# Kernel optimization log

Measured on AMD Instinct MI355X. Metric: run time of the kernel, lower is better.

The kernel has to match this reference:

```python
import jax, jax.numpy as jnp
import numpy as np

DIM = 1024
DIM_HEAD = 64
HEADS = 8
MULT = 4
ATTN_INNER = HEADS * DIM_HEAD            # 512
FF_INNER = MULT * DIM                    # 4096
FUSED = ATTN_INNER + DIM_HEAD + DIM_HEAD + 2 * FF_INNER  # 8832


def setup_inputs() -> dict:
    key = jax.random.key(0)
    ks = jax.random.split(key, 5)
    x = jax.random.normal(ks[0], (2, 2048, DIM), dtype=jnp.float32)
    gamma = jnp.ones((DIM,), dtype=jnp.float32)
    # Linear weights stored as [in, out]
    w_fused = jax.random.normal(ks[1], (DIM, FUSED), dtype=jnp.float32) * (DIM ** -0.5)
    w_attn_out = jax.random.normal(ks[2], (ATTN_INNER, DIM), dtype=jnp.float32) * (ATTN_INNER ** -0.5)
    w_ff_out = jax.random.normal(ks[3], (FF_INNER, DIM), dtype=jnp.float32) * (FF_INNER ** -0.5)
    return {"x": x, "gamma": gamma, "w_fused": w_fused,
            "w_attn_out": w_attn_out, "w_ff_out": w_ff_out}


def _forward(x, gamma, w_fused, w_attn_out, w_ff_out):
    b, n, d = x.shape
    # LayerNorm (beta buffer is zeros)
    mu = jnp.mean(x, axis=-1, keepdims=True)
    var = jnp.mean(jnp.square(x - mu), axis=-1, keepdims=True)
    xn = (x - mu) * jax.lax.rsqrt(var + 1e-5) * gamma
    # fused QKV + FF projection
    proj = jnp.einsum('bnd,df->bnf', xn, w_fused)
    q = proj[..., :ATTN_INNER]
    k = proj[..., ATTN_INNER:ATTN_INNER + DIM_HEAD]
    v = proj[..., ATTN_INNER + DIM_HEAD:ATTN_INNER + 2 * DIM_HEAD]
    ff = proj[..., ATTN_INNER + 2 * DIM_HEAD:]
    # multi-query attention: single shared K/V head of width DIM_HEAD
    q = q.reshape(b, n, HEADS, DIM_HEAD).transpose(0, 2, 1, 3) * (DIM_HEAD ** -0.5)
    sim = jnp.einsum('bhid,bjd->bhij', q, k)
    attn = jax.nn.softmax(sim, axis=-1)
    out = jnp.einsum('bhij,bjd->bhid', attn, v)
    out = out.transpose(0, 2, 1, 3).reshape(b, n, ATTN_INNER)
    attn_out = jnp.einsum('bna,ad->bnd', out, w_attn_out)
    # parallel SwiGLU FF: chunk -> (x_part, gate); silu(gate)*x_part
    ff_x, gate = ff[..., :FF_INNER], ff[..., FF_INNER:]
    ff_out = jnp.einsum('bnf,fd->bnd', jax.nn.silu(gate) * ff_x, w_ff_out)
    return attn_out + ff_out


def reference(x, gamma, w_fused, w_attn_out, w_ff_out):
    return _forward(x, gamma, w_fused, w_attn_out, w_ff_out)
```

## Files before the change

kernel.cpp:

```cpp
#include <hip/hip_runtime.h>
#include <hip/hip_bf16.h>
#include <stdint.h>

#define DIM     1024
#define SEQ     2048
#define NTOK    4096
#define HEADS   8
#define DH      64
#define AINNER  512
#define FFI     4096
#define FUSED   8832
#define HCOLS   4608

typedef __attribute__((ext_vector_type(8))) short short8;
typedef __attribute__((ext_vector_type(4))) short short4v;
typedef __attribute__((ext_vector_type(4))) float f32x4;

__device__ __forceinline__ short f2bf(float f) {
  union { float f; uint32_t u; } v; v.f = f;
  uint32_t r = v.u + 0x7fffu + ((v.u >> 16) & 1u);
  return (short)(r >> 16);
}
__device__ __forceinline__ float bf2f(short s) {
  union { uint32_t u; float f; } v; v.u = ((uint32_t)(uint16_t)s) << 16;
  return v.f;
}
__device__ __forceinline__ void g2l16(const void* g, void* l) {
  __builtin_amdgcn_global_load_lds((const __attribute__((address_space(1))) void*)g,
                                   (__attribute__((address_space(3))) void*)l, 16, 0, 0);
}

__global__ __launch_bounds__(256) void k_transpose_wf(const float* __restrict__ src,
                                                      short* __restrict__ dst) {
  __shared__ short tile[32][33];
  int c0 = blockIdx.x * 32;
  int r0 = blockIdx.y * 32;
  int tx = threadIdx.x & 31, ty = threadIdx.x >> 5;
#pragma unroll
  for (int i = 0; i < 32; i += 8)
    tile[ty + i][tx] = f2bf(src[(size_t)(r0 + ty + i) * FUSED + c0 + tx]);
  __syncthreads();
#pragma unroll
  for (int i = 0; i < 32; i += 8)
    dst[(size_t)(c0 + ty + i) * DIM + r0 + tx] = tile[tx][ty + i];
}

__global__ __launch_bounds__(256) void k_transpose_w2(const float* __restrict__ wao,
                                                      const float* __restrict__ wfo,
                                                      short* __restrict__ dst) {
  __shared__ short tile[32][33];
  int c0 = blockIdx.x * 32;
  int r0 = blockIdx.y * 32;
  int tx = threadIdx.x & 31, ty = threadIdx.x >> 5;
#pragma unroll
  for (int i = 0; i < 32; i += 8) {
    int r = r0 + ty + i;
    float v = (r < AINNER) ? wao[(size_t)r * DIM + c0 + tx]
                           : wfo[(size_t)(r - AINNER) * DIM + c0 + tx];
    tile[ty + i][tx] = f2bf(v);
  }
  __syncthreads();
#pragma unroll
  for (int i = 0; i < 32; i += 8)
    dst[(size_t)(c0 + ty + i) * HCOLS + r0 + tx] = tile[tx][ty + i];
}

__global__ __launch_bounds__(256) void k_ln(const float* __restrict__ x,
                                            const float* __restrict__ gamma,
                                            short* __restrict__ xn) {
  int row = blockIdx.x;
  int t = threadIdx.x;
  const float4* xr = (const float4*)(x + (size_t)row * DIM);
  float4 v = xr[t];
  float s = v.x + v.y + v.z + v.w;
  float s2 = v.x * v.x + v.y * v.y + v.z * v.z + v.w * v.w;
#pragma unroll
  for (int m = 1; m < 64; m <<= 1) { s += __shfl_xor(s, m); s2 += __shfl_xor(s2, m); }
  __shared__ float red[8];
  int w = t >> 6;
  if ((t & 63) == 0) { red[w] = s; red[4 + w] = s2; }
  __syncthreads();
  s = red[0] + red[1] + red[2] + red[3];
  s2 = red[4] + red[5] + red[6] + red[7];
  float mu = s * (1.f / DIM);
  float rs = rsqrtf(s2 * (1.f / DIM) - mu * mu + 1e-5f);
  const float4* g4 = (const float4*)gamma;
  float4 g = g4[t];
  short4v o;
  o.x = f2bf((v.x - mu) * rs * g.x);
  o.y = f2bf((v.y - mu) * rs * g.y);
  o.z = f2bf((v.z - mu) * rs * g.z);
  o.w = f2bf((v.w - mu) * rs * g.w);
  ((short4v*)(xn + (size_t)row * DIM))[t] = o;
}

template <int MODE, int BN>
__global__ __launch_bounds__(512, 2) void gemm8(const short* __restrict__ A, int lda,
                                                const short* __restrict__ Bt, int ldb,
                                                int K, void* __restrict__ out0,
                                                void* __restrict__ out1,
                                                void* __restrict__ out2,
                                                void* __restrict__ out3) {
  extern __shared__ __align__(16) short S[];
  constexpr int NFR = BN / 64;
  constexpr int BHALF = (BN == 256) ? 8192 : 4096;
  int tid = threadIdx.x, l = tid & 63, w = tid >> 6;
  int wm = w >> 2, wn = w & 3;
  int gx = gridDim.x, nwg = gx * gridDim.y;
  int hw = blockIdx.y * gx + blockIdx.x;
  int qq = nwg >> 3;
  int tile = (hw & 7) * qq + (hw >> 3);
  int bx = tile % gx, by = tile / gx;
  int mBase = by * 256, nBase = bx * BN;

  int srow = w * 8 + (l >> 3);
  int cs = (l & 7) ^ (l >> 3);
  const short* Ag = A + (size_t)(mBase + srow) * lda + cs * 8;
  const short* Bg = Bt + (size_t)(nBase + srow) * ldb + cs * 8;
  int dsto = w * 512 + l * 8;

#define STAGE_ALL(kt, db2)                                                      \
  {                                                                             \
    _Pragma("unroll") for (int h = 0; h < 2; ++h)                               \
        _Pragma("unroll") for (int s2 = 0; s2 < 2; ++s2)                        \
            g2l16(Ag + (size_t)(h * 128 + s2 * 64) * lda + (kt) * 64,           \
                  S + ((db2) * 2 + h) * 8192 + s2 * 4096 + dsto);               \
    if constexpr (BN == 256) {                                                  \
      _Pragma("unroll") for (int h = 0; h < 2; ++h)                             \
          _Pragma("unroll") for (int s2 = 0; s2 < 2; ++s2)                      \
              g2l16(Bg + (size_t)(h * 128 + s2 * 64) * ldb + (kt) * 64,         \
                    S + 32768 + ((db2) * 2 + h) * 8192 + s2 * 4096 + dsto);     \
    } else {                                                                    \
      _Pragma("unroll") for (int h = 0; h < 2; ++h)                             \
          g2l16(Bg + (size_t)(h * 64) * ldb + (kt) * 64,                        \
                S + 32768 + ((db2) * 2 + h) * 4096 + dsto);                     \
    }                                                                           \
  }

  int NT = K >> 6;
  STAGE_ALL(0, 0);

  int c0 = l & 15, kg = l >> 4, cx = l & 7;
  int brow = (wn & 1) * (BN / 4);
  f32x4 zero = {0.f, 0.f, 0.f, 0.f};
  f32x4 acc[8][NFR];
#pragma unroll
  for (int m = 0; m < 8; ++m)
#pragma unroll
    for (int n = 0; n < NFR; ++n) acc[m][n] = zero;

  for (int kt = 0; kt < NT; ++kt) {
    int db = kt & 1, dbn = db ^ 1;
    asm volatile("s_waitcnt vmcnt(0)\ns_barrier" ::: "memory");
    if (kt + 1 < NT) STAGE_ALL(kt + 1, dbn);
    const short* Ab = S + (db * 2 + wm) * 8192;
    const short* Bb = S + 32768 + (db * 2 + (wn >> 1)) * BHALF;
#pragma unroll
    for (int kkh = 0; kkh < 2; ++kkh) {
      int ch = (kkh * 4 + kg) ^ cx;
      short8 b[NFR], a[8];
#pragma unroll
      for (int n = 0; n < NFR; ++n)
        b[n] = *(const short8*)(Bb + (brow + n * 16 + c0) * 64 + ch * 8);
#pragma unroll
      for (int m = 0; m < 8; ++m)
        a[m] = *(const short8*)(Ab + (m * 16 + c0) * 64 + ch * 8);
      __builtin_amdgcn_s_setprio(1);
#pragma unroll
      for (int m = 0; m < 8; ++m)
#pragma unroll
        for (int n = 0; n < NFR; ++n)
          acc[m][n] = __builtin_amdgcn_mfma_f32_16x16x32_bf16(a[m], b[n], acc[m][n], 0, 0, 0);
      __builtin_amdgcn_s_setprio(0);
    }
  }
#undef STAGE_ALL

  int r0 = (l >> 4) * 4;
#pragma unroll
  for (int m = 0; m < 8; ++m)
#pragma unroll
    for (int n = 0; n < NFR; ++n)
#pragma unroll
      for (int r = 0; r < 4; ++r) {
        float val = acc[m][n][r];
        int row = mBase + wm * 128 + m * 16 + r0 + r;
        int col = nBase + wn * (BN / 4) + n * 16 + c0;
        if (MODE == 0) {
          if (col < AINNER)
            ((short*)out0)[(size_t)row * AINNER + col] = f2bf(val);
          else if (col < AINNER + DH)
            ((short*)out1)[(size_t)row * DH + (col - AINNER)] = f2bf(val);
          else if (col < AINNER + 2 * DH)
            ((short*)out2)[((size_t)(row >> 11) * DH + (col - AINNER - DH)) * SEQ +
                           (row & (SEQ - 1))] = f2bf(val);
          else
            ((short*)out3)[(size_t)row * HCOLS + AINNER + (col - 640)] = f2bf(val);
        } else {
          short* Hp = (short*)out0;
          size_t idx = (size_t)row * HCOLS + AINNER + col;
          float sg = val / (1.f + __expf(-val));
          Hp[idx] = f2bf(sg * bf2f(Hp[idx]));
        }
      }
}

__global__ __launch_bounds__(512, 2) void gemm_r(const short* __restrict__ A, int lda,
                                                 const short* __restrict__ Bt, int ldb,
                                                 int K, float* __restrict__ out0) {
  extern __shared__ __align__(16) short SA[];
  int tid = threadIdx.x, l = tid & 63, w = tid >> 6;
  int gx = gridDim.x;
  int nwg = gx * gridDim.y;
  int hw = blockIdx.y * gx + blockIdx.x;
  int qq = nwg >> 3;
  int tile = (hw & 7) * qq + (hw >> 3);
  int bx = tile % gx, by = tile / gx;
  int mBase = by * 128, nBase = bx * 128;

  int srow = w * 8 + (l >> 3);
  int cs = (l & 7) ^ (l >> 3);
  const short* Ag = A + (size_t)(mBase + srow) * lda + cs * 8;
  const short* Bg = Bt + (size_t)(nBase + srow) * ldb + cs * 8;
  short* ldsA = SA + w * 512 + l * 8;
  short* ldsB = ldsA + 8192;

  int NT = K >> 6;
  for (int tt = 0; tt < 3; ++tt) {
    int slot = tt & 3;
#pragma unroll
    for (int i = 0; i < 2; ++i) {
      g2l16(Ag + (size_t)(i * 64) * lda + tt * 64, ldsA + slot * 16384 + i * 4096);
      g2l16(Bg + (size_t)(i * 64) * ldb + tt * 64, ldsB + slot * 16384 + i * 4096);
    }
  }

  int wr = w >> 2, wc = w & 3;
  int c0 = l & 15, kg = l >> 4, cx = l & 7;
  f32x4 zero = {0.f, 0.f, 0.f, 0.f};
  f32x4 acc[4][2];
#pragma unroll
  for (int m = 0; m < 4; ++m)
#pragma unroll
    for (int n = 0; n < 2; ++n) acc[m][n] = zero;

  for (int kt = 0; kt < NT; ++kt) {
    if (kt + 2 < NT)      asm volatile("s_waitcnt vmcnt(8)\ns_barrier" ::: "memory");
    else if (kt + 1 < NT) asm volatile("s_waitcnt vmcnt(4)\ns_barrier" ::: "memory");
    else                  asm volatile("s_waitcnt vmcnt(0)\ns_barrier" ::: "memory");
    int slot = kt & 3;
    const short* Ab = SA + slot * 16384;
    const short* Bb = Ab + 8192;
    short8 af[4][2], bfr[2][2];
#pragma unroll
    for (int m = 0; m < 4; ++m)
#pragma unroll
      for (int kk = 0; kk < 2; ++kk)
        af[m][kk] = *(const short8*)(Ab + (wr * 64 + m * 16 + c0) * 64 + ((kk * 4 + kg) ^ cx) * 8);
#pragma unroll
    for (int n = 0; n < 2; ++n)
#pragma unroll
      for (int kk = 0; kk < 2; ++kk)
        bfr[n][kk] = *(const short8*)(Bb + (wc * 32 + n * 16 + c0) * 64 + ((kk * 4 + kg) ^ cx) * 8);
    int ts = kt + 3;
    if (ts < NT) {
      int s2 = ts & 3;
#pragma unroll
      for (int i = 0; i < 2; ++i) {
        g2l16(Ag + (size_t)(i * 64) * lda + ts * 64, ldsA + s2 * 16384 + i * 4096);
        g2l16(Bg + (size_t)(i * 64) * ldb + ts * 64, ldsB + s2 * 16384 + i * 4096);
      }
    }
    __builtin_amdgcn_s_setprio(1);
#pragma unroll
    for (int m = 0; m < 4; ++m)
#pragma unroll
      for (int n = 0; n < 2; ++n)
#pragma unroll
        for (int kk = 0; kk < 2; ++kk)
          acc[m][n] = __builtin_amdgcn_mfma_f32_16x16x32_bf16(af[m][kk], bfr[n][kk],
                                                              acc[m][n], 0, 0, 0);
    __builtin_amdgcn_s_setprio(0);
  }

  int r0 = (l >> 4) * 4;
#pragma unroll
  for (int m = 0; m < 4; ++m)
#pragma unroll
    for (int n = 0; n < 2; ++n)
#pragma unroll
      for (int r = 0; r < 4; ++r) {
        int row = mBase + wr * 64 + m * 16 + r0 + r;
        int col = nBase + wc * 32 + n * 16 + c0;
        out0[(size_t)row * DIM + col] = acc[m][n][r];
      }
}

__global__ __launch_bounds__(256) void k_attn(const short* __restrict__ qb,
                                              const short* __restrict__ kb,
                                              const short* __restrict__ vt,
                                              short* __restrict__ H) {
  __shared__ __align__(16) short Qs[64 * 64];
  __shared__ __align__(16) short Ks[128 * 64];
  __shared__ __align__(16) short Vs[64 * 128];
  __shared__ __align__(16) short Ps[4][16 * 128];
  int t = threadIdx.x, l = t & 63, w = t >> 6;
  int qt = blockIdx.x, bh = blockIdx.y;
  int b = bh >> 3, h = bh & 7;
  int q0 = qt * 64;

  int srow = w * 8 + (l >> 3);
  int schunk = (l & 7) ^ (l >> 3);
  {
    const short* Qg = qb + (size_t)(b * SEQ + q0 + srow) * AINNER + h * DH + schunk * 8;
    short* qs = Qs + w * 512 + l * 8;
#pragma unroll
    for (int i = 0; i < 2; ++i) g2l16(Qg + (size_t)(i * 32) * AINNER, qs + i * 2048);
  }
  const short* Kg = kb + (size_t)(b * SEQ + srow) * DH + schunk * 8;
  short* ksl = Ks + w * 512 + l * 8;
  int vrow = w * 4 + (l >> 4);
  int vchunk = (l & 15) ^ (vrow & 7);
  const short* Vg = vt + (size_t)b * DH * SEQ + (size_t)vrow * SEQ + vchunk * 8;
  short* vsl = Vs + w * 512 + l * 8;

#pragma unroll
  for (int i = 0; i < 4; ++i) {
    g2l16(Kg + (size_t)(i * 32) * DH, ksl + i * 2048);
    g2l16(Vg + (size_t)(i * 16) * SEQ, vsl + i * 2048);
  }

  float m_run[4], l_run[4];
  f32x4 zero = {0.f, 0.f, 0.f, 0.f};
  f32x4 Oacc[4];
#pragma unroll
  for (int r = 0; r < 4; ++r) { m_run[r] = -1e30f; l_run[r] = 0.f; }
#pragma unroll
  for (int n = 0; n < 4; ++n) Oacc[n] = zero;

  int c0 = l & 15, kg = l >> 4, cx = l & 7;
  short* pw = Ps[w];

  for (int kv0 = 0; kv0 < SEQ; kv0 += 128) {
    asm volatile("s_waitcnt vmcnt(0)\ns_barrier" ::: "memory");

    f32x4 sacc[8];
#pragma unroll
    for (int n = 0; n < 8; ++n) sacc[n] = zero;
#pragma unroll
    for (int kk = 0; kk < 2; ++kk) {
      int rr = w * 16 + c0;
      short8 aq = *(const short8*)(Qs + rr * 64 + ((kk * 4 + kg) ^ cx) * 8);
#pragma unroll
      for (int n = 0; n < 8; ++n) {
        int kr = n * 16 + c0;
        short8 bk = *(const short8*)(Ks + kr * 64 + ((kk * 4 + kg) ^ cx) * 8);
        sacc[n] = __builtin_amdgcn_mfma_f32_16x16x32_bf16(aq, bk, sacc[n], 0, 0, 0);
      }
    }
#pragma unroll
    for (int r = 0; r < 4; ++r) {
      float mx = -1e30f;
#pragma unroll
      for (int n = 0; n < 8; ++n) {
        sacc[n][r] *= 0.125f;
        mx = fmaxf(mx, sacc[n][r]);
      }
#pragma unroll
      for (int msk = 1; msk < 16; msk <<= 1) mx = fmaxf(mx, __shfl_xor(mx, msk));
      float nm = fmaxf(m_run[r], mx);
      float corr = __expf(m_run[r] - nm);
      m_run[r] = nm;
      float rs = 0.f;
#pragma unroll
      for (int n = 0; n < 8; ++n) {
        float p = __expf(sacc[n][r] - nm);
        sacc[n][r] = p;
        rs += p;
      }
#pragma unroll
      for (int msk = 1; msk < 16; msk <<= 1) rs += __shfl_xor(rs, msk);
      l_run[r] = l_run[r] * corr + rs;
      Oacc[0][r] *= corr; Oacc[1][r] *= corr; Oacc[2][r] *= corr; Oacc[3][r] *= corr;
    }
#pragma unroll
    for (int n = 0; n < 8; ++n)
#pragma unroll
      for (int r = 0; r < 4; ++r) {
        int pr = (l >> 4) * 4 + r;
        int pc = n * 16 + c0;
        pw[pr * 128 + ((pc >> 3) ^ (pr & 7)) * 8 + (pc & 7)] = f2bf(sacc[n][r]);
      }
    asm volatile("s_waitcnt lgkmcnt(0)" ::: "memory");
#pragma unroll
    for (int kk = 0; kk < 4; ++kk) {
      int pr = c0;
      short8 ap = *(const short8*)(pw + pr * 128 + ((kk * 4 + kg) ^ cx) * 8);
#pragma unroll
      for (int n = 0; n < 4; ++n) {
        int vr = n * 16 + c0;
        short8 bv = *(const short8*)(Vs + vr * 128 + ((kk * 4 + kg) ^ (vr & 7)) * 8);
        Oacc[n] = __builtin_amdgcn_mfma_f32_16x16x32_bf16(ap, bv, Oacc[n], 0, 0, 0);
      }
    }
    __syncthreads();
    int nx = kv0 + 128;
    if (nx < SEQ) {
#pragma unroll
      for (int i = 0; i < 4; ++i) {
        g2l16(Kg + (size_t)(nx + i * 32) * DH, ksl + i * 2048);
        g2l16(Vg + nx + (size_t)(i * 16) * SEQ, vsl + i * 2048);
      }
    }
  }
#pragma unroll
  for (int r = 0; r < 4; ++r) {
    float inv = 1.f / l_run[r];
    int row = b * SEQ + q0 + w * 16 + (l >> 4) * 4 + r;
#pragma unroll
    for (int n = 0; n < 4; ++n) {
      int col = h * DH + n * 16 + c0;
      H[(size_t)row * HCOLS + col] = f2bf(Oacc[n][r] * inv);
    }
  }
}

extern "C" void kernel_launch(void* const* d_in, const int* in_sizes, int n_in,
                              void* d_out, int out_size, void* d_ws, size_t ws_size,
                              hipStream_t stream) {
  const float* x     = (const float*)d_in[0];
  const float* gamma = (const float*)d_in[1];
  const float* w_f   = (const float*)d_in[2];
  const float* w_ao  = (const float*)d_in[3];
  const float* w_fo  = (const float*)d_in[4];
  float* out = (float*)d_out;

  char* ws = (char*)d_ws;
  size_t o = 0;
  short* WtF = (short*)(ws + o); o += (size_t)FUSED * DIM * 2;
  short* Wt2 = (short*)(ws + o); o += (size_t)DIM * HCOLS * 2;
  short* xn  = (short*)(ws + o); o += (size_t)NTOK * DIM * 2;
  short* qb  = (short*)(ws + o); o += (size_t)NTOK * AINNER * 2;
  short* kbf = (short*)(ws + o); o += (size_t)NTOK * DH * 2;
  short* vtb = (short*)(ws + o); o += (size_t)NTOK * DH * 2;
  short* H   = (short*)(ws + o); o += (size_t)NTOK * HCOLS * 2;

  k_transpose_wf<<<dim3(FUSED / 32, DIM / 32), 256, 0, stream>>>(w_f, WtF);
  k_transpose_w2<<<dim3(DIM / 32, HCOLS / 32), 256, 0, stream>>>(w_ao, w_fo, Wt2);
  k_ln<<<NTOK, 256, 0, stream>>>(x, gamma, xn);
  gemm8<0, 128><<<dim3(37, 16), 512, 98304, stream>>>(xn, DIM, WtF, DIM, DIM,
                                                      qb, kbf, vtb, H);
  k_attn<<<dim3(32, 16), 256, 0, stream>>>(qb, kbf, vtb, H);
  gemm8<1, 256><<<dim3(16, 16), 512, 131072, stream>>>(xn, DIM, WtF + (size_t)4736 * DIM, DIM,
                                                       DIM, H, nullptr, nullptr, nullptr);
  gemm_r<<<dim3(8, 32), 512, 131072, stream>>>(H, HCOLS, Wt2, HCOLS, HCOLS, out);
}
```

Measured before the change: 231.9 us.

## Fuse SwiGLU gate into projection GEMM and split-K the output GEMM

Measured after the change: 223.4 us. 3.7% less time.

```diff
diff --git a/kernel.cpp b/kernel.cpp
--- a/kernel.cpp
+++ b/kernel.cpp
@@ -94,115 +94,209 @@
   ((short4v*)(xn + (size_t)row * DIM))[t] = o;
 }
 
-template <int MODE, int BN>
-__global__ __launch_bounds__(512, 2) void gemm8(const short* __restrict__ A, int lda,
-                                                const short* __restrict__ Bt, int ldb,
-                                                int K, void* __restrict__ out0,
-                                                void* __restrict__ out1,
-                                                void* __restrict__ out2,
-                                                void* __restrict__ out3) {
+__global__ __launch_bounds__(512, 2) void p1(const short* __restrict__ A,
+                                             const short* __restrict__ Bt,
+                                             short* __restrict__ qb,
+                                             short* __restrict__ kbf,
+                                             short* __restrict__ vtb,
+                                             short* __restrict__ H) {
   extern __shared__ __align__(16) short S[];
-  constexpr int NFR = BN / 64;
-  constexpr int BHALF = (BN == 256) ? 8192 : 4096;
   int tid = threadIdx.x, l = tid & 63, w = tid >> 6;
   int wm = w >> 2, wn = w & 3;
-  int gx = gridDim.x, nwg = gx * gridDim.y;
-  int hw = blockIdx.y * gx + blockIdx.x;
-  int qq = nwg >> 3;
-  int tile = (hw & 7) * qq + (hw >> 3);
-  int bx = tile % gx, by = tile / gx;
-  int mBase = by * 256, nBase = bx * BN;
+  int hw = blockIdx.y * 37 + blockIdx.x;
+  int tile = (hw & 7) * 74 + (hw >> 3);
+  int bx = tile % 37, by = tile / 37;
+  int mBase = by * 256;
+  bool fused = bx < 32;
+  int b0row = fused ? (640 + bx * 128) : ((bx - 32) * 128);
+  int b1row = 4736 + bx * 128;
 
   int srow = w * 8 + (l >> 3);
   int cs = (l & 7) ^ (l >> 3);
-  const short* Ag = A + (size_t)(mBase + srow) * lda + cs * 8;
-  const short* Bg = Bt + (size_t)(nBase + srow) * ldb + cs * 8;
+  const short* Ag = A + (size_t)(mBase + srow) * DIM + cs * 8;
+  const short* Bg0 = Bt + (size_t)(b0row + srow) * DIM + cs * 8;
+  const short* Bg1 = Bt + (size_t)(b1row + srow) * DIM + cs * 8;
   int dsto = w * 512 + l * 8;
 
-#define STAGE_ALL(kt, db2)                                                      \
+#define P1_STAGE(kt, db)                                                        \
   {                                                                             \
-    _Pragma("unroll") for (int h = 0; h < 2; ++h)                               \
-        _Pragma("unroll") for (int s2 = 0; s2 < 2; ++s2)                        \
-            g2l16(Ag + (size_t)(h * 128 + s2 * 64) * lda + (kt) * 64,           \
-                  S + ((db2) * 2 + h) * 8192 + s2 * 4096 + dsto);               \
-    if constexpr (BN == 256) {                                                  \
-      _Pragma("unroll") for (int h = 0; h < 2; ++h)                             \
-          _Pragma("unroll") for (int s2 = 0; s2 < 2; ++s2)                      \
-              g2l16(Bg + (size_t)(h * 128 + s2 * 64) * ldb + (kt) * 64,         \
-                    S + 32768 + ((db2) * 2 + h) * 8192 + s2 * 4096 + dsto);     \
-    } else {                                                                    \
-      _Pragma("unroll") for (int h = 0; h < 2; ++h)                             \
-          g2l16(Bg + (size_t)(h * 64) * ldb + (kt) * 64,                        \
-                S + 32768 + ((db2) * 2 + h) * 4096 + dsto);                     \
+    _Pragma("unroll") for (int i = 0; i < 4; ++i)                               \
+        g2l16(Ag + (size_t)(i * 64) * DIM + (kt) * 64,                          \
+              S + (db) * 16384 + i * 4096 + dsto);                              \
+    _Pragma("unroll") for (int i = 0; i < 2; ++i)                               \
+        g2l16(Bg0 + (size_t)(i * 64) * DIM + (kt) * 64,                         \
+              S + 32768 + (db) * 16384 + i * 4096 + dsto);                      \
+    if (fused) {                                                                \
+      _Pragma("unroll") for (int i = 0; i < 2; ++i)                             \
+          g2l16(Bg1 + (size_t)(i * 64) * DIM + (kt) * 64,                       \
+                S + 32768 + (db) * 16384 + 8192 + i * 4096 + dsto);             \
     }                                                                           \
   }
 
-  int NT = K >> 6;
-  STAGE_ALL(0, 0);
+  const int NT = DIM / 64;
+  P1_STAGE(0, 0);
 
   int c0 = l & 15, kg = l >> 4, cx = l & 7;
-  int brow = (wn & 1) * (BN / 4);
   f32x4 zero = {0.f, 0.f, 0.f, 0.f};
-  f32x4 acc[8][NFR];
+  f32x4 accF[8][2], accG[8][2];
 #pragma unroll
   for (int m = 0; m < 8; ++m)
 #pragma unroll
-    for (int n = 0; n < NFR; ++n) acc[m][n] = zero;
+    for (int n = 0; n < 2; ++n) { accF[m][n] = zero; accG[m][n] = zero; }
 
   for (int kt = 0; kt < NT; ++kt) {
     int db = kt & 1, dbn = db ^ 1;
     asm volatile("s_waitcnt vmcnt(0)\ns_barrier" ::: "memory");
-    if (kt + 1 < NT) STAGE_ALL(kt + 1, dbn);
-    const short* Ab = S + (db * 2 + wm) * 8192;
-    const short* Bb = S + 32768 + (db * 2 + (wn >> 1)) * BHALF;
+    if (kt + 1 < NT) P1_STAGE(kt + 1, dbn);
+    const short* Ab = S + db * 16384;
+    const short* Bb = S + 32768 + db * 16384;
 #pragma unroll
     for (int kkh = 0; kkh < 2; ++kkh) {
-      int ch = (kkh * 4 + kg) ^ cx;
-      short8 b[NFR], a[8];
-#pragma unroll
-      for (int n = 0; n < NFR; ++n)
-        b[n] = *(const short8*)(Bb + (brow + n * 16 + c0) * 64 + ch * 8);
-#pragma unroll
-      for (int m = 0; m < 8; ++m)
-        a[m] = *(const short8*)(Ab + (m * 16 + c0) * 64 + ch * 8);
+      int ch8 = ((kkh * 4 + kg) ^ cx) * 8;
+      short8 bf0 = *(const short8*)(Bb + (wn * 32 + c0) * 64 + ch8);
+      short8 bf1 = *(const short8*)(Bb + (wn * 32 + 16 + c0) * 64 + ch8);
+      if (fused) {
+        short8 bg0 = *(const short8*)(Bb + (128 + wn * 32 + c0) * 64 + ch8);
+        short8 bg1 = *(const short8*)(Bb + (128 + wn * 32 + 16 + c0) * 64 + ch8);
+        __builtin_amdgcn_s_setprio(1);
+#pragma unroll
+        for (int m = 0; m < 8; ++m) {
+          short8 a = *(const short8*)(Ab + (wm * 128 + m * 16 + c0) * 64 + ch8);
+          accF[m][0] = __builtin_amdgcn_mfma_f32_16x16x32_bf16(a, bf0, accF[m][0], 0, 0, 0);
+          accF[m][1] = __builtin_amdgcn_mfma_f32_16x16x32_bf16(a, bf1, accF[m][1], 0, 0, 0);
+          accG[m][0] = __builtin_amdgcn_mfma_f32_16x16x32_bf16(a, bg0, accG[m][0], 0, 0, 0);
+          accG[m][1] = __builtin_amdgcn_mfma_f32_16x16x32_bf16(a, bg1, accG[m][1], 0, 0, 0);
+        }
+        __builtin_amdgcn_s_setprio(0);
+      } else {
+        __builtin_amdgcn_s_setprio(1);
+#pragma unroll
+        for (int m = 0; m < 8; ++m) {
+          short8 a = *(const short8*)(Ab + (wm * 128 + m * 16 + c0) * 64 + ch8);
+          accF[m][0] = __builtin_amdgcn_mfma_f32_16x16x32_bf16(a, bf0, accF[m][0], 0, 0, 0);
+          accF[m][1] = __builtin_amdgcn_mfma_f32_16x16x32_bf16(a, bf1, accF[m][1], 0, 0, 0);
+        }
+        __builtin_amdgcn_s_setprio(0);
+      }
+    }
+  }
+#undef P1_STAGE
+
+  int r0 = (l >> 4) * 4;
+#pragma unroll
+  for (int m = 0; m < 8; ++m)
+#pragma unroll
+    for (int n = 0; n < 2; ++n)
+#pragma unroll
+      for (int r = 0; r < 4; ++r) {
+        int row = mBase + wm * 128 + m * 16 + r0 + r;
+        if (fused) {
+          int col = bx * 128 + wn * 32 + n * 16 + c0;
+          float g = accG[m][n][r];
+          float sg = g / (1.f + __expf(-g));
+          H[(size_t)row * HCOLS + AINNER + col] = f2bf(sg * accF[m][n][r]);
+        } else {
+          int col = (bx - 32) * 128 + wn * 32 + n * 16 + c0;
+          float val = accF[m][n][r];
+          if (col < AINNER)
+            qb[(size_t)row * AINNER + col] = f2bf(val);
+          else if (col < AINNER + DH)
+            kbf[(size_t)row * DH + (col - AINNER)] = f2bf(val);
+          else
+            vtb[((size_t)(row >> 11) * DH + (col - AINNER - DH)) * SEQ +
+                (row & (SEQ - 1))] = f2bf(val);
+        }
+      }
+}
+
+__global__ __launch_bounds__(512, 2) void gemm_s(const short* __restrict__ A,
+                                                 const short* __restrict__ Bt,
+                                                 short* __restrict__ part) {
+  extern __shared__ __align__(16) short S[];
+  int tid = threadIdx.x, l = tid & 63, w = tid >> 6;
+  int wm = w >> 2, wn = w & 3;
+  int hw = (blockIdx.z * 16 + blockIdx.y) * 4 + blockIdx.x;
+  int tile = (hw & 7) * 32 + (hw >> 3);
+  int bx = tile & 3, by = (tile >> 2) & 15, bz = tile >> 6;
+  int mBase = by * 256, nBase = bx * 256;
+  int kOff = bz * 1152;
+
+  int srow = w * 8 + (l >> 3);
+  int cs = (l & 7) ^ (l >> 3);
+  const short* Ag = A + (size_t)(mBase + srow) * HCOLS + kOff + cs * 8;
+  const short* Bg = Bt + (size_t)(nBase + srow) * HCOLS + kOff + cs * 8;
+  int dsto = w * 512 + l * 8;
+
+#define GS_STAGE(kt, db)                                                        \
+  {                                                                             \
+    _Pragma("unroll") for (int i = 0; i < 4; ++i) {                             \
+      g2l16(Ag + (size_t)(i * 64) * HCOLS + (kt) * 64,                          \
+            S + (db) * 16384 + i * 4096 + dsto);                                \
+      g2l16(Bg + (size_t)(i * 64) * HCOLS + (kt) * 64,                          \
+            S + 32768 + (db) * 16384 + i * 4096 + dsto);                        \
+    }                                                                           \
+  }
+
+  const int NT = 18;
+  GS_STAGE(0, 0);
+
+  int c0 = l & 15, kg = l >> 4, cx = l & 7;
+  f32x4 zero = {0.f, 0.f, 0.f, 0.f};
+  f32x4 acc[8][4];
+#pragma unroll
+  for (int m = 0; m < 8; ++m)
+#pragma unroll
+    for (int n = 0; n < 4; ++n) acc[m][n] = zero;
+
+  for (int kt = 0; kt < NT; ++kt) {
+    int db = kt & 1, dbn = db ^ 1;
+    asm volatile("s_waitcnt vmcnt(0)\ns_barrier" ::: "memory");
+    if (kt + 1 < NT) GS_STAGE(kt + 1, dbn);
+    const short* Ab = S + db * 16384;
+    const short* Bb = S + 32768 + db * 16384;
+#pragma unroll
+    for (int kkh = 0; kkh < 2; ++kkh) {
+      int ch8 = ((kkh * 4 + kg) ^ cx) * 8;
+      short8 b[4];
+#pragma unroll
+      for (int n = 0; n < 4; ++n)
+        b[n] = *(const short8*)(Bb + (wn * 64 + n * 16 + c0) * 64 + ch8);
       __builtin_amdgcn_s_setprio(1);
 #pragma unroll
-      for (int m = 0; m < 8; ++m)
-#pragma unroll
-        for (int n = 0; n < NFR; ++n)
-          acc[m][n] = __builtin_amdgcn_mfma_f32_16x16x32_bf16(a[m], b[n], acc[m][n], 0, 0, 0);
+      for (int m = 0; m < 8; ++m) {
+        short8 a = *(const short8*)(Ab + (wm * 128 + m * 16 + c0) * 64 + ch8);
+#pragma unroll
+        for (int n = 0; n < 4; ++n)
+          acc[m][n] = __builtin_amdgcn_mfma_f32_16x16x32_bf16(a, b[n], acc[m][n], 0, 0, 0);
+      }
       __builtin_amdgcn_s_setprio(0);
     }
   }
-#undef STAGE_ALL
+#undef GS_STAGE
 
   int r0 = (l >> 4) * 4;
 #pragma unroll
   for (int m = 0; m < 8; ++m)
 #pragma unroll
-    for (int n = 0; n < NFR; ++n)
+    for (int n = 0; n < 4; ++n)
 #pragma unroll
       for (int r = 0; r < 4; ++r) {
-        float val = acc[m][n][r];
         int row = mBase + wm * 128 + m * 16 + r0 + r;
-        int col = nBase + wn * (BN / 4) + n * 16 + c0;
-        if (MODE == 0) {
-          if (col < AINNER)
-            ((short*)out0)[(size_t)row * AINNER + col] = f2bf(val);
-          else if (col < AINNER + DH)
-            ((short*)out1)[(size_t)row * DH + (col - AINNER)] = f2bf(val);
-          else if (col < AINNER + 2 * DH)
-            ((short*)out2)[((size_t)(row >> 11) * DH + (col - AINNER - DH)) * SEQ +
-                           (row & (SEQ - 1))] = f2bf(val);
-          else
-            ((short*)out3)[(size_t)row * HCOLS + AINNER + (col - 640)] = f2bf(val);
-        } else {
-          short* Hp = (short*)out0;
-          size_t idx = (size_t)row * HCOLS + AINNER + col;
-          float sg = val / (1.f + __expf(-val));
-          Hp[idx] = f2bf(sg * bf2f(Hp[idx]));
-        }
-      }
+        int col = nBase + wn * 64 + n * 16 + c0;
+        part[(size_t)bz * (NTOK * DIM) + (size_t)row * DIM + col] = f2bf(acc[m][n][r]);
+      }
+}
+
+__global__ __launch_bounds__(256) void k_red(const short* __restrict__ part,
+                                             float* __restrict__ out) {
+  int i = (blockIdx.x * 256 + threadIdx.x) * 4;
+  float4 s = {0.f, 0.f, 0.f, 0.f};
+#pragma unroll
+  for (int ks = 0; ks < 4; ++ks) {
+    short4v v = *(const short4v*)(part + (size_t)ks * (NTOK * DIM) + i);
+    s.x += bf2f(v.x); s.y += bf2f(v.y); s.z += bf2f(v.z); s.w += bf2f(v.w);
+  }
+  *(float4*)(out + i) = s;
 }
 
 __global__ __launch_bounds__(512, 2) void gemm_r(const short* __restrict__ A, int lda,
@@ -444,14 +538,18 @@
   short* kbf = (short*)(ws + o); o += (size_t)NTOK * DH * 2;
   short* vtb = (short*)(ws + o); o += (size_t)NTOK * DH * 2;
   short* H   = (short*)(ws + o); o += (size_t)NTOK * HCOLS * 2;
+  short* part = (short*)(ws + o);
+  size_t need = o + (size_t)4 * NTOK * DIM * 2;
 
   k_transpose_wf<<<dim3(FUSED / 32, DIM / 32), 256, 0, stream>>>(w_f, WtF);
   k_transpose_w2<<<dim3(DIM / 32, HCOLS / 32), 256, 0, stream>>>(w_ao, w_fo, Wt2);
   k_ln<<<NTOK, 256, 0, stream>>>(x, gamma, xn);
-  gemm8<0, 128><<<dim3(37, 16), 512, 98304, stream>>>(xn, DIM, WtF, DIM, DIM,
-                                                      qb, kbf, vtb, H);
+  p1<<<dim3(37, 16), 512, 131072, stream>>>(xn, WtF, qb, kbf, vtb, H);
   k_attn<<<dim3(32, 16), 256, 0, stream>>>(qb, kbf, vtb, H);
-  gemm8<1, 256><<<dim3(16, 16), 512, 131072, stream>>>(xn, DIM, WtF + (size_t)4736 * DIM, DIM,
-                                                       DIM, H, nullptr, nullptr, nullptr);
-  gemm_r<<<dim3(8, 32), 512, 131072, stream>>>(H, HCOLS, Wt2, HCOLS, HCOLS, out);
-}
+  if (ws_size >= need) {
+    gemm_s<<<dim3(4, 16, 4), 512, 131072, stream>>>(H, Wt2, part);
+    k_red<<<NTOK * DIM / 1024, 256, 0, stream>>>(part, out);
+  } else {
+    gemm_r<<<dim3(8, 32), 512, 131072, stream>>>(H, HCOLS, Wt2, HCOLS, HCOLS, out);
+  }
+}
```
